# Kernel optimization log

Hardware: AMD Instinct MI355X
Metric: run time of the kernel (lower is better)

## Reference

```python
import jax, jax.numpy as jnp
import numpy as np
import math

B, S, H, W, C = 8, 16, 512, 512, 1
NT, WIN, SIGMA, ITERS = 256, 21, 2.0, 5
K = WIN * WIN

_SOBEL_X = jnp.array([[-1., 0., 1.], [-2., 0., 2.], [-1., 0., 1.]], jnp.float32).reshape(3, 3, 1, 1)
_SOBEL_Y = jnp.array([[-1., -2., -1.], [0., 0., 0.], [1., 2., 1.]], jnp.float32).reshape(3, 3, 1, 1)


def _win_weights():
    c = WIN // 2
    yy, xx = np.mgrid[0:WIN, 0:WIN]
    d = np.sqrt((xx - c) ** 2 + (yy - c) ** 2)
    g = 1.0 / (SIGMA * math.sqrt(2 * math.pi)) * np.exp(-0.5 * (d / SIGMA) ** 2)
    return jnp.asarray(g.reshape(K), dtype=jnp.float32)


def _sampling_grid():
    lin = jnp.linspace(-1.0, 1.0, WIN)
    x_t, y_t = jnp.meshgrid(lin, lin)  # 'xy' indexing, matches tf.meshgrid
    return jnp.stack([x_t.reshape(-1), y_t.reshape(-1)])  # [2, K]


def _bilinear(sampler, frames2):
    # sampler [B,NT,2,K]; frames2 [B,2,H,W] -> samples [B,2,NT,K]
    x = sampler[:, :, 0] * (WIN * 0.5)  # [B,NT,K] pixel coords
    y = sampler[:, :, 1] * (WIN * 0.5)
    x0 = jnp.clip(jnp.floor(x), 0, W - 1)
    x1 = jnp.clip(jnp.floor(x) + 1, 0, W - 1)
    y0 = jnp.clip(jnp.floor(y), 0, H - 1)
    y1 = jnp.clip(jnp.floor(y) + 1, 0, H - 1)
    wa = (y1 - y) * (x1 - x)
    wb = (y1 - y) * (x - x0)
    wc = (y - y0) * (x1 - x)
    wd = (y - y0) * (x - x0)
    flat = frames2.reshape(frames2.shape[0], 2, H * W)

    def gat(yi, xi):
        idx = (yi.astype(jnp.int32) * W + xi.astype(jnp.int32)).reshape(yi.shape[0], 1, -1)
        idx = jnp.broadcast_to(idx, (yi.shape[0], 2, idx.shape[-1]))
        return jnp.take_along_axis(flat, idx, axis=2).reshape(-1, 2, NT, K)

    Ia, Ib, Ic, Id = gat(y0, x0), gat(y0, x1), gat(y1, x0), gat(y1, x1)
    return (wa[:, None] * Ia + wb[:, None] * Ib + wc[:, None] * Ic + wd[:, None] * Id)


def _calc_velocity(first, second, ww):
    # first/second [B,NT,K] windows; LK 2x2 normal-equation solve per track
    img = first.reshape(-1, WIN, WIN, 1)
    dn = ('NHWC', 'HWIO', 'NHWC')
    Ix = jax.lax.conv_general_dilated(img, _SOBEL_X, (1, 1), 'SAME', dimension_numbers=dn).reshape(-1, NT, K)
    Iy = jax.lax.conv_general_dilated(img, _SOBEL_Y, (1, 1), 'SAME', dimension_numbers=dn).reshape(-1, NT, K)
    A = jnp.stack([Ix, Iy], axis=-1)  # [B,NT,K,2]
    ATA = jnp.einsum('bnki,bnkj->bnij', A, A * ww[None, None, :, None])
    a, b = ATA[..., 0, 0], ATA[..., 0, 1]
    c, d = ATA[..., 1, 0], ATA[..., 1, 1]
    inv_det = 1.0 / (a * d - b * c + 1e-7)
    bvec = -(second - first) * ww  # [B,NT,K]
    ATb = jnp.einsum('bnki,bnk->bni', A, bvec)
    vx = inv_det * (d * ATb[..., 0] - b * ATb[..., 1])
    vy = inv_det * (-c * ATb[..., 0] + a * ATb[..., 1])
    return jnp.stack([vx, vy], axis=-1)  # [B,NT,2]


def _iterative_lk(sampler, frames2, ww):
    out = _bilinear(sampler, frames2)
    first = out[:, 0]
    v = _calc_velocity(first, out[:, 1], ww)
    sampler = sampler + v[..., None]
    sum_v = v
    for _ in range(ITERS - 1):
        out = _bilinear(sampler, frames2)
        v = _calc_velocity(first, out[:, 1], ww)
        sampler = sampler + v[..., None]
        sum_v = sum_v + v
    return sampler, sum_v


def setup_inputs() -> dict:
    key = jax.random.key(0)
    k1, k2 = jax.random.split(key)
    track_locs = jax.random.uniform(k1, (B, NT, 2), dtype=jnp.float32)
    imgs = jax.random.uniform(k2, (B, S, H, W, C), dtype=jnp.float32)
    return {"track_locs": track_locs, "imgs": imgs}


def reference(track_locs, imgs):
    imgs2 = imgs[..., 0]  # [B,S,H,W], c==1
    cr = jnp.array([W / WIN, H / WIN], jnp.float32)
    ww = _win_weights()
    init = track_locs.reshape(-1, NT, 2) * cr + cr  # [B,NT,2]
    sampler = init[..., None] + _sampling_grid()[None, None]  # [B,NT,2,K]
    sampler, sv = _iterative_lk(sampler, imgs2[:, 0:2], ww)
    pos0 = init
    pos1 = init + sv
    fa = jnp.moveaxis(imgs2[:, 1:S - 1], 1, 0)  # [S-2,B,H,W]
    fb = jnp.moveaxis(imgs2[:, 2:S], 1, 0)

    def step(carry, x):
        smp, prev = carry
        frames2 = jnp.stack(x, axis=1)  # [B,2,H,W]
        smp, svv = _iterative_lk(smp, frames2, ww)
        pos = prev + svv
        return (smp, pos), pos

    _, poss = jax.lax.scan(step, (sampler, pos1), (fa, fb))
    tot = jnp.concatenate([pos0[None], pos1[None], poss], axis=0)  # [S,B,NT,2]
    tot = jnp.transpose(tot, (1, 2, 0, 3))  # [B,NT,S,2]
    return (tot - cr) / cr
```

## Files before the change

kernel.cpp:

```cpp
#pragma clang fp contract(off)
#include <hip/hip_runtime.h>
#include <math.h>


#define WINSZ 21
#define KPTS  441
#define NPT   7
#define PSTR  452

struct SB {
  float fw[23][24];
  float pqT[6][PSTR];
};

__device__ __forceinline__ float bilinf(const float* __restrict__ F,
                                        float x, float y) {
  #pragma clang fp contract(off)
  float fx = floorf(x), fy = floorf(y);
  float x0 = fminf(fmaxf(fx, 0.0f), 511.0f);
  float x1a = fx + 1.0f;
  float x1 = fminf(fmaxf(x1a, 0.0f), 511.0f);
  float y0 = fminf(fmaxf(fy, 0.0f), 511.0f);
  float y1a = fy + 1.0f;
  float y1 = fminf(fmaxf(y1a, 0.0f), 511.0f);
  float dy1 = y1 - y, dx1 = x1 - x, dy0 = y - y0, dx0 = x - x0;
  float wa = dy1 * dx1;
  float wb = dy1 * dx0;
  float wc = dy0 * dx1;
  float wd = dy0 * dx0;
  int jx0 = (int)x0, jx1 = (int)x1, jy0 = (int)y0, jy1 = (int)y1;
  float Ia = F[jy0 * 512 + jx0];
  float Ib = F[jy0 * 512 + jx1];
  float Ic = F[jy1 * 512 + jx0];
  float Id = F[jy1 * 512 + jx1];
  float pA = wa * Ia;
  float pB = wb * Ib;
  float pC = wc * Ic;
  float pD = wd * Id;
  float s = pA + pB;
  s = s + pC;
  s = s + pD;
  return s;
}

__global__ __launch_bounds__(64) void lk_track(
    const float* __restrict__ track_locs,
    const float* __restrict__ imgs,
    float* __restrict__ out)
{
  #pragma clang fp contract(off)
  __shared__ SB S;
  const float CRF = (float)(512.0 / 21.0);
  const int SS = 16, HW = 512 * 512;

  const int tr   = blockIdx.x;
  const int b    = tr >> 8;
  const int lane = threadIdx.x;

  for (int i = lane; i < 23 * 24; i += 64) (&S.fw[0][0])[i] = 0.0f;

  const bool act = (lane < 63);
  int   rr[NPT], cc[NPT];
  float gxv[NPT], gyv[NPT], wwv[NPT];
  const double gnorm = 1.0 / (2.0 * sqrt(2.0 * 3.141592653589793));
#pragma unroll
  for (int j = 0; j < NPT; j++) {
    int k = lane * NPT + j;
    if (k >= KPTS) k = 0;
    int r = k / WINSZ, c = k % WINSZ;
    rr[j] = r; cc[j] = c;
    gxv[j] = (c == 20) ? 1.0f : (float)((double)c * 0.1 - 1.0);
    gyv[j] = (r == 20) ? 1.0f : (float)((double)r * 0.1 - 1.0);
    double dd = sqrt((double)((c - 10) * (c - 10) + (r - 10) * (r - 10)));
    double q  = dd / 2.0;
    wwv[j] = (float)(gnorm * exp(-0.5 * (q * q)));
  }

  const float* tl = track_locs + (size_t)tr * 2;
  float mx = tl[0] * CRF; float initx = mx + CRF;
  float my = tl[1] * CRF; float inity = my + CRF;

  float sx[NPT], sy[NPT];
#pragma unroll
  for (int j = 0; j < NPT; j++) { sx[j] = initx + gxv[j]; sy[j] = inity + gyv[j]; }

  float px = initx, py = inity;
  if (lane == 0) {
    float* o = out + (size_t)tr * SS * 2;
    float n0 = initx - CRF; o[0] = n0 / CRF;
    float n1 = inity - CRF; o[1] = n1 / CRF;
  }

  int g6 = lane >> 3; if (g6 > 5) g6 = g6 - 2;
  const int grp2 = lane >> 5;
  const float* row6 = &S.pqT[g6][0];
  const float* rowB = &S.pqT[4 + grp2][0];

  float fv[NPT], scv[NPT], ixv[NPT], iyv[NPT];

  for (int t = 0; t < SS - 1; t++) {
    const float* F0 = imgs + ((size_t)b * SS + t) * HW;
    const float* F1 = F0 + HW;

    __syncthreads();
#pragma unroll
    for (int j = 0; j < NPT; j++) {
      float x = sx[j] * 10.5f, y = sy[j] * 10.5f;
      fv[j]  = bilinf(F0, x, y);
      scv[j] = bilinf(F1, x, y);
      if (act) S.fw[rr[j] + 1][cc[j] + 1] = fv[j];
    }
    __syncthreads();

#pragma unroll
    for (int j = 0; j < NPT; j++) {
      int r = rr[j], c = cc[j];
      float a00 = S.fw[r][c],     a01 = S.fw[r][c + 1],     a02 = S.fw[r][c + 2];
      float a10 = S.fw[r + 1][c],                           a12 = S.fw[r + 1][c + 2];
      float a20 = S.fw[r + 2][c], a21 = S.fw[r + 2][c + 1], a22 = S.fw[r + 2][c + 2];
      float xc0 = -a00;
      float xc1 = 2.0f * a12;
      float xc2 = a02 + (-a20);
      float xc3 = -2.0f * a10;
      float xh0 = xc0 + xc1;
      float xh1 = xc2 + xc3;
      float Ix = xh0 + xh1;
      Ix = Ix + a22;
      float yc0 = -a00;
      float yc1 = -2.0f * a01;
      float yc2 = (-a02) + a20;
      float yc3 = 2.0f * a21;
      float yh0 = yc0 + yc1;
      float yh1 = yc2 + yc3;
      float Iy = yh0 + yh1;
      Iy = Iy + a22;
      ixv[j] = Ix; iyv[j] = Iy;
      if (act) {
        int k = lane * NPT + j;
        float tx = Ix * wwv[j];
        float ty = Iy * wwv[j];
        float p0 = Ix * tx;
        float p1 = Ix * ty;
        float p2 = Iy * tx;
        float p3 = Iy * ty;
        S.pqT[0][k] = p0;
        S.pqT[1][k] = p1;
        S.pqT[2][k] = p2;
        S.pqT[3][k] = p3;
        float d2 = fv[j] - scv[j];
        float bw = d2 * wwv[j];
        float u0 = ixv[j] * bw;
        float u1 = iyv[j] * bw;
        S.pqT[4][k] = u0;
        S.pqT[5][k] = u1;
      }
    }
    __syncthreads();

    float acc = 0.f;
#pragma unroll 11
    for (int m = 0; m < 110; m++) {
      float4 v = *reinterpret_cast<const float4*>(&row6[4 * m]);
      acc = acc + v.x;
      acc = acc + v.y;
      acc = acc + v.z;
      acc = acc + v.w;
    }
    acc = acc + row6[440];
    float aa = __shfl(acc, 0,  64);
    float bb = __shfl(acc, 8,  64);
    float cN = __shfl(acc, 16, 64);
    float dN = __shfl(acc, 24, 64);
    float s0 = __shfl(acc, 32, 64);
    float s1 = __shfl(acc, 40, 64);
    float q0 = aa * dN;
    float q1 = bb * cN;
    float det = q0 - q1;
    det = det + 1e-7f;
    float inv_det = 1.0f / det;

    float svx = 0.f, svy = 0.f;
    for (int it = 0; it < 5; it++) {
      if (it > 0) {
#pragma unroll
        for (int j = 0; j < NPT; j++) {
          float x = sx[j] * 10.5f, y = sy[j] * 10.5f;
          scv[j] = bilinf(F1, x, y);
        }
#pragma unroll
        for (int j = 0; j < NPT; j++) {
          if (act) {
            int k = lane * NPT + j;
            float d2 = fv[j] - scv[j];
            float bw = d2 * wwv[j];
            float u0 = ixv[j] * bw;
            float u1 = iyv[j] * bw;
            S.pqT[4][k] = u0;
            S.pqT[5][k] = u1;
          }
        }
        __syncthreads();
        float accB = 0.f;
#pragma unroll 11
        for (int m = 0; m < 110; m++) {
          float4 v = *reinterpret_cast<const float4*>(&rowB[4 * m]);
          accB = accB + v.x;
          accB = accB + v.y;
          accB = accB + v.z;
          accB = accB + v.w;
        }
        accB = accB + rowB[440];
        s0 = __shfl(accB, 0,  64);
        s1 = __shfl(accB, 32, 64);
      }
      float e0 = dN * s0;
      float e1 = bb * s1;
      float numx = e0 - e1;
      float vx = inv_det * numx;
      float f0 = (-cN) * s0;
      float f1 = aa * s1;
      float numy = f0 + f1;
      float vy = inv_det * numy;
#pragma unroll
      for (int j = 0; j < NPT; j++) { sx[j] = sx[j] + vx; sy[j] = sy[j] + vy; }
      if (it == 0) { svx = vx;       svy = vy; }
      else         { svx = svx + vx; svy = svy + vy; }
      __syncthreads();
    }

    px = px + svx; py = py + svy;
    if (lane == 0) {
      float* o = out + ((size_t)tr * SS + (t + 1)) * 2;
      float n0 = px - CRF; o[0] = n0 / CRF;
      float n1 = py - CRF; o[1] = n1 / CRF;
    }
  }
}

extern "C" void kernel_launch(void* const* d_in, const int* in_sizes, int n_in,
                              void* d_out, int out_size, void* d_ws, size_t ws_size,
                              hipStream_t stream) {
  const float* tl   = (const float*)d_in[0];
  const float* imgs = (const float*)d_in[1];
  float* o          = (float*)d_out;
  lk_track<<<dim3(2048), dim3(64), 0, stream>>>(tl, imgs, o);
}
```

Baseline: 384.1 us.

## Stage bounding-box image patch in LDS before bilinear sampling

Computes a wave-wide bounding box of the sample coordinates and, when it fits in a 24x24 region inside the image, cooperatively loads that patch of both frames into shared memory. Bilinear gathers then read from LDS instead of scattered global loads, and a fallback keeps the original global path. This aims to replace many uncoalesced global gathers (four per sample per frame) with coalesced patch loads, at the cost of extra reductions, syncs and shared memory.

```diff
diff --git a/kernel.cpp b/kernel.cpp
--- a/kernel.cpp
+++ b/kernel.cpp
@@ -7,10 +7,14 @@
 #define KPTS  441
 #define NPT   7
 #define PSTR  452
+#define RDIM  24
+#define RPX   576
 
 struct SB {
   float fw[23][24];
   float pqT[6][PSTR];
+  float regA[RPX];
+  float regB[RPX];
 };
 
 __device__ __forceinline__ float bilinf(const float* __restrict__ F,
@@ -43,6 +47,38 @@
   return s;
 }
 
+__device__ __forceinline__ void wcalc(float x, float y, int cb,
+                                      float* w, int* idx) {
+  #pragma clang fp contract(off)
+  float fx = floorf(x), fy = floorf(y);
+  float x1 = fx + 1.0f;
+  float y1 = fy + 1.0f;
+  float dy1 = y1 - y, dx1 = x1 - x, dy0 = y - fy, dx0 = x - fx;
+  w[0] = dy1 * dx1;
+  w[1] = dy1 * dx0;
+  w[2] = dy0 * dx1;
+  w[3] = dy0 * dx0;
+  int ix0 = (int)fx, iy0 = (int)fy;
+  *idx = iy0 * RDIM + ix0 - cb;
+}
+
+__device__ __forceinline__ float rsum(const float* __restrict__ reg,
+                                      const float* w, int idx) {
+  #pragma clang fp contract(off)
+  float Ia = reg[idx];
+  float Ib = reg[idx + 1];
+  float Ic = reg[idx + RDIM];
+  float Id = reg[idx + RDIM + 1];
+  float pA = w[0] * Ia;
+  float pB = w[1] * Ib;
+  float pC = w[2] * Ic;
+  float pD = w[3] * Id;
+  float s = pA + pB;
+  s = s + pC;
+  s = s + pD;
+  return s;
+}
+
 __global__ __launch_bounds__(64) void lk_track(
     const float* __restrict__ track_locs,
     const float* __restrict__ imgs,
@@ -76,6 +112,15 @@
     wwv[j] = (float)(gnorm * exp(-0.5 * (q * q)));
   }
 
+  int soff[9];
+#pragma unroll
+  for (int i = 0; i < 9; i++) {
+    int f = lane + 64 * i;
+    int r = f / RDIM;
+    int c = f - RDIM * r;
+    soff[i] = r * 512 + c;
+  }
+
   const float* tl = track_locs + (size_t)tr * 2;
   float mx = tl[0] * CRF; float initx = mx + CRF;
   float my = tl[1] * CRF; float inity = my + CRF;
@@ -103,12 +148,56 @@
     const float* F1 = F0 + HW;
 
     __syncthreads();
-#pragma unroll
-    for (int j = 0; j < NPT; j++) {
-      float x = sx[j] * 10.5f, y = sy[j] * 10.5f;
-      fv[j]  = bilinf(F0, x, y);
-      scv[j] = bilinf(F1, x, y);
-      if (act) S.fw[rr[j] + 1][cc[j] + 1] = fv[j];
+
+    float xmn = sx[0], xmx = sx[0], ymn = sy[0], ymx = sy[0];
+#pragma unroll
+    for (int j = 1; j < NPT; j++) {
+      xmn = fminf(xmn, sx[j]); xmx = fmaxf(xmx, sx[j]);
+      ymn = fminf(ymn, sy[j]); ymx = fmaxf(ymx, sy[j]);
+    }
+#pragma unroll
+    for (int m = 32; m >= 1; m >>= 1) {
+      xmn = fminf(xmn, __shfl_xor(xmn, m, 64));
+      xmx = fmaxf(xmx, __shfl_xor(xmx, m, 64));
+      ymn = fminf(ymn, __shfl_xor(ymn, m, 64));
+      ymx = fmaxf(ymx, __shfl_xor(ymx, m, 64));
+    }
+    float xminp = xmn * 10.5f, xmaxp = xmx * 10.5f;
+    float yminp = ymn * 10.5f, ymaxp = ymx * 10.5f;
+    float bxf = floorf(xminp), byf = floorf(yminp);
+    bool fast = (bxf >= 0.0f) && (byf >= 0.0f) &&
+                (bxf <= 488.0f) && (byf <= 488.0f) &&
+                (xmaxp < bxf + 23.0f) && (ymaxp < byf + 23.0f);
+    int bx = 0, by = 0, gbase = 0, cb = 0;
+    if (fast) {
+      bx = (int)bxf; by = (int)byf;
+      gbase = by * 512 + bx;
+      cb = by * RDIM + bx;
+    }
+
+    if (fast) {
+#pragma unroll
+      for (int i = 0; i < 9; i++) S.regA[lane + 64 * i] = F0[gbase + soff[i]];
+#pragma unroll
+      for (int i = 0; i < 9; i++) S.regB[lane + 64 * i] = F1[gbase + soff[i]];
+      __syncthreads();
+#pragma unroll
+      for (int j = 0; j < NPT; j++) {
+        float x = sx[j] * 10.5f, y = sy[j] * 10.5f;
+        float w[4]; int id;
+        wcalc(x, y, cb, w, &id);
+        fv[j]  = rsum(S.regA, w, id);
+        scv[j] = rsum(S.regB, w, id);
+        if (act) S.fw[rr[j] + 1][cc[j] + 1] = fv[j];
+      }
+    } else {
+#pragma unroll
+      for (int j = 0; j < NPT; j++) {
+        float x = sx[j] * 10.5f, y = sy[j] * 10.5f;
+        fv[j]  = bilinf(F0, x, y);
+        scv[j] = bilinf(F1, x, y);
+        if (act) S.fw[rr[j] + 1][cc[j] + 1] = fv[j];
+      }
     }
     __syncthreads();
 
@@ -182,10 +271,45 @@
     float svx = 0.f, svy = 0.f;
     for (int it = 0; it < 5; it++) {
       if (it > 0) {
-#pragma unroll
-        for (int j = 0; j < NPT; j++) {
-          float x = sx[j] * 10.5f, y = sy[j] * 10.5f;
-          scv[j] = bilinf(F1, x, y);
+        float xmn2 = sx[0], xmx2 = sx[0], ymn2 = sy[0], ymx2 = sy[0];
+#pragma unroll
+        for (int j = 1; j < NPT; j++) {
+          xmn2 = fminf(xmn2, sx[j]); xmx2 = fmaxf(xmx2, sx[j]);
+          ymn2 = fminf(ymn2, sy[j]); ymx2 = fmaxf(ymx2, sy[j]);
+        }
+#pragma unroll
+        for (int m = 32; m >= 1; m >>= 1) {
+          xmn2 = fminf(xmn2, __shfl_xor(xmn2, m, 64));
+          xmx2 = fmaxf(xmx2, __shfl_xor(xmx2, m, 64));
+          ymn2 = fminf(ymn2, __shfl_xor(ymn2, m, 64));
+          ymx2 = fmaxf(ymx2, __shfl_xor(ymx2, m, 64));
+        }
+        float xminp2 = xmn2 * 10.5f, xmaxp2 = xmx2 * 10.5f;
+        float yminp2 = ymn2 * 10.5f, ymaxp2 = ymx2 * 10.5f;
+        float bxf2 = floorf(xminp2), byf2 = floorf(yminp2);
+        bool fast2 = (bxf2 >= 0.0f) && (byf2 >= 0.0f) &&
+                     (bxf2 <= 488.0f) && (byf2 <= 488.0f) &&
+                     (xmaxp2 < bxf2 + 23.0f) && (ymaxp2 < byf2 + 23.0f);
+        if (fast2) {
+          int bx2 = (int)bxf2, by2 = (int)byf2;
+          int gbase2 = by2 * 512 + bx2;
+          int cb2 = by2 * RDIM + bx2;
+#pragma unroll
+          for (int i = 0; i < 9; i++) S.regB[lane + 64 * i] = F1[gbase2 + soff[i]];
+          __syncthreads();
+#pragma unroll
+          for (int j = 0; j < NPT; j++) {
+            float x = sx[j] * 10.5f, y = sy[j] * 10.5f;
+            float w[4]; int id;
+            wcalc(x, y, cb2, w, &id);
+            scv[j] = rsum(S.regB, w, id);
+          }
+        } else {
+#pragma unroll
+          for (int j = 0; j < NPT; j++) {
+            float x = sx[j] * 10.5f, y = sy[j] * 10.5f;
+            scv[j] = bilinf(F1, x, y);
+          }
         }
 #pragma unroll
         for (int j = 0; j < NPT; j++) {
```

Result: faster. 344.7 us (-10.2%).
